# Optimization experiments

Hardware: AMD Instinct MI355X
Metric: run time of the kernel (lower is better)

## Reference

```python
import jax, jax.numpy as jnp
import numpy as np

IN_DIM = 128
D_MODEL = 2 * IN_DIM        # 256, Mamba d_model
D_INNER = 2 * D_MODEL       # 512, expand=2
D_STATE = 16
D_CONV = 4
DT_RANK = (D_MODEL + 15) // 16  # 16
B = 4
C = 1024                    # original channel dim -> Mamba sequence length
EPS = 1e-5


def rmsnorm(x, w):
    return x * jax.lax.rsqrt(jnp.mean(x * x, axis=-1, keepdims=True) + EPS) * w


def conv1x1(x, w, b):
    # x: (B, Cin, L); 1x1 conv == channel matmul
    return jnp.einsum('oi,bil->bol', w, x) + b[None, :, None]


def mamba(u, in_w, conv_w, conv_b, xproj_w, dt_w, dt_b, A_log, Dp, out_w):
    # u: (B, L, D_MODEL) -- faithful mamba_ssm Mamba block (defaults)
    di, K = conv_w.shape
    n = A_log.shape[1]
    r = dt_w.shape[1]
    xz = u @ in_w.T                              # (B,L,2*di)
    xx, z = jnp.split(xz, 2, axis=-1)
    # depthwise causal conv over L
    xt = jnp.pad(jnp.transpose(xx, (0, 2, 1)), ((0, 0), (0, 0), (K - 1, 0)))
    xc = jax.lax.conv_general_dilated(xt, conv_w[:, None, :], (1,), 'VALID',
                                      feature_group_count=di)
    xx = jax.nn.silu(jnp.transpose(xc + conv_b[None, :, None], (0, 2, 1)))
    dbl = xx @ xproj_w.T                         # (B,L,r+2n)
    dt, Bm, Cm = dbl[..., :r], dbl[..., r:r + n], dbl[..., r + n:]
    dt = jax.nn.softplus(dt @ dt_w.T + dt_b)     # (B,L,di)
    A = -jnp.exp(A_log)                          # (di,n)
    dA = jnp.exp(dt[..., None] * A)              # (B,L,di,n)
    dBx = (dt * xx)[..., None] * Bm[:, :, None, :]

    def step(h, inps):
        dA_t, dBx_t, C_t = inps
        h = dA_t * h + dBx_t
        return h, jnp.einsum('bdn,bn->bd', h, C_t)

    h0 = jnp.zeros((u.shape[0], di, n), u.dtype)
    _, ys = jax.lax.scan(step, h0, (jnp.moveaxis(dA, 1, 0),
                                    jnp.moveaxis(dBx, 1, 0),
                                    jnp.moveaxis(Cm, 1, 0)))
    y = jnp.moveaxis(ys, 0, 1) + xx * Dp
    return (y * jax.nn.silu(z)) @ out_w.T


def postnorm_mamba(u, params, norm_w):
    return rmsnorm(mamba(u, *params), norm_w) + u


def _forward(x, W_in, b_in, W_wp, b_wp, W_fp, b_fp, W_bp, b_bp, W_out, b_out,
             norm_w_top,
             f_in_w, f_conv_w, f_conv_b, f_xproj_w, f_dt_w, f_dt_b, f_A_log, f_D, f_out_w, f_norm_w,
             bk_in_w, bk_conv_w, bk_conv_b, bk_xproj_w, bk_dt_w, bk_dt_b, bk_A_log, bk_D, bk_out_w, bk_norm_w):
    residual = x                                  # (B, C, L)
    xn = rmsnorm(x, norm_w_top)                   # RMSNorm over L
    xt = jnp.transpose(xn, (0, 2, 1))             # (B, L, C); L acts as conv channels
    ssm_in = conv1x1(xt, W_in, b_in)              # (B, 2L, C)
    # forward branch
    fwd = conv1x1(ssm_in, W_fp, b_fp)
    fwd = jnp.transpose(fwd, (0, 2, 1))           # (B, C, 2L): Mamba seq=C
    fwd = postnorm_mamba(fwd, (f_in_w, f_conv_w, f_conv_b, f_xproj_w, f_dt_w,
                               f_dt_b, f_A_log, f_D, f_out_w), f_norm_w)
    fwd = jnp.transpose(fwd, (0, 2, 1))           # (B, 2L, C)
    # backward branch (flip along C)
    bwd = conv1x1(ssm_in[:, :, ::-1], W_bp, b_bp)
    bwd = jnp.transpose(bwd, (0, 2, 1))
    bwd = postnorm_mamba(bwd, (bk_in_w, bk_conv_w, bk_conv_b, bk_xproj_w, bk_dt_w,
                               bk_dt_b, bk_A_log, bk_D, bk_out_w), bk_norm_w)
    bwd = jnp.transpose(bwd, (0, 2, 1))[:, :, ::-1]
    # swish gate
    w = conv1x1(xt, W_wp, b_wp)
    w = w * jax.nn.sigmoid(w)
    out = conv1x1(w * fwd + w * bwd, W_out, b_out)  # (B, L, C)
    return jnp.transpose(out, (0, 2, 1)) + residual  # (B, C, L)


def setup_inputs():
    key = jax.random.key(0)
    ks = iter(jax.random.split(key, 64))
    rn = lambda shape, s=0.02: jax.random.normal(next(ks), shape, jnp.float32) * s
    inp = {"x": jax.random.normal(next(ks), (B, C, IN_DIM), jnp.float32)}
    inp["W_in"] = rn((2 * IN_DIM, IN_DIM));   inp["b_in"] = rn((2 * IN_DIM,), 0.1)
    inp["W_wp"] = rn((2 * IN_DIM, IN_DIM));   inp["b_wp"] = rn((2 * IN_DIM,), 0.1)
    inp["W_fp"] = rn((2 * IN_DIM, 2 * IN_DIM)); inp["b_fp"] = rn((2 * IN_DIM,), 0.1)
    inp["W_bp"] = rn((2 * IN_DIM, 2 * IN_DIM)); inp["b_bp"] = rn((2 * IN_DIM,), 0.1)
    inp["W_out"] = rn((IN_DIM, 2 * IN_DIM));  inp["b_out"] = rn((IN_DIM,), 0.1)
    inp["norm_w_top"] = jnp.ones((IN_DIM,), jnp.float32)
    A_init = jnp.log(jnp.broadcast_to(jnp.arange(1, D_STATE + 1, dtype=jnp.float32),
                                      (D_INNER, D_STATE)))
    for p in ("f", "bk"):
        inp[p + "_in_w"] = rn((2 * D_INNER, D_MODEL))
        inp[p + "_conv_w"] = rn((D_INNER, D_CONV), 0.2)
        inp[p + "_conv_b"] = rn((D_INNER,), 0.1)
        inp[p + "_xproj_w"] = rn((DT_RANK + 2 * D_STATE, D_INNER))
        inp[p + "_dt_w"] = rn((D_INNER, DT_RANK), 0.1)
        inp[p + "_dt_b"] = rn((D_INNER,), 0.5)
        inp[p + "_A_log"] = A_init
        inp[p + "_D"] = jnp.ones((D_INNER,), jnp.float32)
        inp[p + "_out_w"] = rn((D_MODEL, D_INNER))
        inp[p + "_norm_w"] = jnp.ones((D_MODEL,), jnp.float32)
    return inp


def reference(x, W_in, b_in, W_wp, b_wp, W_fp, b_fp, W_bp, b_bp, W_out, b_out,
              norm_w_top,
              f_in_w, f_conv_w, f_conv_b, f_xproj_w, f_dt_w, f_dt_b, f_A_log, f_D, f_out_w, f_norm_w,
              bk_in_w, bk_conv_w, bk_conv_b, bk_xproj_w, bk_dt_w, bk_dt_b, bk_A_log, bk_D, bk_out_w, bk_norm_w):
    return _forward(x, W_in, b_in, W_wp, b_wp, W_fp, b_fp, W_bp, b_bp, W_out, b_out,
                    norm_w_top,
                    f_in_w, f_conv_w, f_conv_b, f_xproj_w, f_dt_w, f_dt_b, f_A_log, f_D, f_out_w, f_norm_w,
                    bk_in_w, bk_conv_w, bk_conv_b, bk_xproj_w, bk_dt_w, bk_dt_b, bk_A_log, bk_D, bk_out_w, bk_norm_w)
```

## Files before the change

kernel.cpp:

```cpp
#include <hip/hip_runtime.h>
#include <math.h>

#define C_LEN 1024
#define NROW 4096
#define NCHUNK 32
#define CHUNK 32

typedef __attribute__((ext_vector_type(8))) short short8;
typedef __attribute__((ext_vector_type(4))) float f32x4;

__device__ __forceinline__ float siluf(float x) { return x / (1.f + __expf(-x)); }

__device__ __forceinline__ unsigned short f2bf(float f) {
    unsigned u = __builtin_bit_cast(unsigned, f);
    unsigned r = (u + 0x7FFFu + ((u >> 16) & 1u)) >> 16;
    return (unsigned short)r;
}
__device__ __forceinline__ float bf2f(unsigned short v) {
    unsigned u = ((unsigned)v) << 16;
    return __builtin_bit_cast(float, u);
}

struct WTab {
    const float* s[6];
    unsigned short* d[6];
    int n[6];
};
__global__ __launch_bounds__(256) void k_prep(WTab t, const float* __restrict__ x,
                                              const float* __restrict__ nw,
                                              unsigned short* __restrict__ xn_bf,
                                              const float* __restrict__ W_fp,
                                              const float* __restrict__ W_bp,
                                              const float* __restrict__ W_in,
                                              const float* __restrict__ b_in,
                                              const float* __restrict__ b_fp,
                                              const float* __restrict__ b_bp,
                                              const float* __restrict__ b_wp,
                                              float* __restrict__ Wpin,
                                              float* __restrict__ bmega,
                                              unsigned short* __restrict__ Wmega) {
    int seg = blockIdx.y;
    if (seg < 6) {
        int n = t.n[seg];
        int i = (blockIdx.x * 256 + threadIdx.x) * 4;
        if (i < n) {
            float4 v = *(const float4*)(t.s[seg] + i);
            unsigned short* o = t.d[seg] + i;
            o[0] = f2bf(v.x); o[1] = f2bf(v.y); o[2] = f2bf(v.z); o[3] = f2bf(v.w);
        }
    } else if (seg == 6) {
        int wave = threadIdx.x >> 6, lane = threadIdx.x & 63;
        #pragma unroll
        for (int it = 0; it < 4; ++it) {
            int row = blockIdx.x * 16 + it * 4 + wave;
            if (row < 4096) {
                float2 v = ((const float2*)(x + (size_t)row * 128))[lane];
                float ss = v.x * v.x + v.y * v.y;
                #pragma unroll
                for (int off = 32; off; off >>= 1) ss += __shfl_xor(ss, off, 64);
                float rs = rsqrtf(ss * (1.f / 128.f) + 1e-5f);
                float2 wv = ((const float2*)nw)[lane];
                ushort2 o;
                o.x = f2bf(v.x * rs * wv.x);
                o.y = f2bf(v.y * rs * wv.y);
                ((ushort2*)(xn_bf + (size_t)row * 128))[lane] = o;
            }
        }
    } else {
        int tg = blockIdx.x * 256 + threadIdx.x;
        if (tg < 65536) {
            int p = tg >> 15, rem = tg & 32767;
            int o = rem >> 7, i = rem & 127;
            const float* Wsrc = p ? W_bp : W_fp;
            float s = 0.f;
            #pragma unroll 8
            for (int j = 0; j < 256; ++j) s += Wsrc[o * 256 + j] * W_in[j * 128 + i];
            Wpin[p * 32768 + o * 128 + i] = s;
            Wmega[(size_t)(p * 256 + o) * 128 + i] = f2bf(s);
        } else if (tg < 66048) {
            int q = tg - 65536;
            int p = q >> 8, o = q & 255;
            const float* Wsrc = p ? W_bp : W_fp;
            const float* badd = p ? b_bp : b_fp;
            float s = badd[o];
            #pragma unroll 8
            for (int j = 0; j < 256; ++j) s += Wsrc[o * 256 + j] * b_in[j];
            bmega[p * 256 + o] = s;
        } else if (tg < 66304) {
            int q = tg - 66048;
            bmega[512 + q] = b_wp[q];
        }
    }
}

__global__ __launch_bounds__(256) void k_wcomb2(const float* __restrict__ f_in_w,
                                                const float* __restrict__ bk_in_w,
                                                const float* __restrict__ Wpin,
                                                unsigned short* __restrict__ Wmega,
                                                float* __restrict__ bmega) {
    int tg = blockIdx.x * 256 + threadIdx.x;
    if (tg < 262144) {
        int p = tg >> 17, rem = tg & 131071;
        int o = rem >> 7, i = rem & 127;
        const float* inw = p ? bk_in_w : f_in_w;
        const float* wp = Wpin + p * 32768;
        float s = 0.f;
        #pragma unroll 8
        for (int j = 0; j < 256; ++j) s += inw[o * 256 + j] * wp[j * 128 + i];
        Wmega[(size_t)(768 + p * 1024 + o) * 128 + i] = f2bf(s);
    } else if (tg < 264192) {
        int q = tg - 262144;
        int p = q >> 10, o = q & 1023;
        const float* inw = p ? bk_in_w : f_in_w;
        const float* bp = bmega + p * 256;
        float s = 0.f;
        #pragma unroll 8
        for (int j = 0; j < 256; ++j) s += inw[o * 256 + j] * bp[j];
        bmega[768 + p * 1024 + o] = s;
    }
}

__global__ __launch_bounds__(256) void k_megagemm(const unsigned short* __restrict__ A,
                                                  const unsigned short* __restrict__ W,
                                                  const float* __restrict__ bias,
                                                  unsigned short* __restrict__ uf,
                                                  unsigned short* __restrict__ ub,
                                                  unsigned short* __restrict__ wbuf,
                                                  unsigned short* __restrict__ xzF,
                                                  unsigned short* __restrict__ xzB) {
    __shared__ __align__(16) unsigned short As[128 * 72];
    __shared__ __align__(16) unsigned short Bs[64 * 72];
    const int K = 128;
    int tid = threadIdx.x;
    int m0 = blockIdx.y * 128, n0 = blockIdx.x * 64;
    int w = tid >> 6, lane = tid & 63;
    int q = lane >> 4, ln = lane & 15;

    unsigned short* Cb; int stride, nc0; bool flip = false, dosilu = false;
    if (n0 < 256)       { Cb = uf;   stride = 256;  nc0 = n0; }
    else if (n0 < 512)  { Cb = ub;   stride = 256;  nc0 = n0 - 256;  flip = true; }
    else if (n0 < 768)  { Cb = wbuf; stride = 256;  nc0 = n0 - 512;  dosilu = true; }
    else if (n0 < 1792) { Cb = xzF;  stride = 1024; nc0 = n0 - 768; }
    else                { Cb = xzB;  stride = 1024; nc0 = n0 - 1792; flip = true; }

    int arow0 = tid >> 1;
    int aseg0 = (tid & 1) * 32;
    int brow = tid >> 2, bseg = (tid & 3) * 16;
    const unsigned short* pa = A + (size_t)(m0 + arow0) * K + aseg0;
    const unsigned short* pw = W + (size_t)(n0 + brow) * K + bseg;

    f32x4 acc[2][4];
    #pragma unroll
    for (int i = 0; i < 2; ++i)
        #pragma unroll
        for (int j = 0; j < 4; ++j) acc[i][j] = (f32x4)(0.f);

    for (int k0 = 0; k0 < K; k0 += 64) {
        #pragma unroll
        for (int h = 0; h < 4; ++h)
            *(short8*)&As[arow0 * 72 + aseg0 + h * 8] = *(const short8*)(pa + h * 8);
        *(short8*)&Bs[brow * 72 + bseg]     = *(const short8*)pw;
        *(short8*)&Bs[brow * 72 + bseg + 8] = *(const short8*)(pw + 8);
        pa += 64; pw += 64;
        __syncthreads();
        short8 a0[2], a1[2];
        #pragma unroll
        for (int i = 0; i < 2; ++i) {
            int row = w * 32 + i * 16 + ln;
            a0[i] = *(const short8*)&As[row * 72 + q * 8];
            a1[i] = *(const short8*)&As[row * 72 + 32 + q * 8];
        }
        #pragma unroll
        for (int j = 0; j < 4; ++j) {
            short8 bf0 = *(const short8*)&Bs[(j * 16 + ln) * 72 + q * 8];
            short8 bf1 = *(const short8*)&Bs[(j * 16 + ln) * 72 + 32 + q * 8];
            #pragma unroll
            for (int i = 0; i < 2; ++i) {
                acc[i][j] = __builtin_amdgcn_mfma_f32_16x16x32_bf16(a0[i], bf0, acc[i][j], 0, 0, 0);
                acc[i][j] = __builtin_amdgcn_mfma_f32_16x16x32_bf16(a1[i], bf1, acc[i][j], 0, 0, 0);
            }
        }
        __syncthreads();
    }
    #pragma unroll
    for (int j = 0; j < 4; ++j) {
        float bsv = bias[n0 + j * 16 + ln];
        int nc = nc0 + j * 16 + ln;
        #pragma unroll
        for (int i = 0; i < 2; ++i) {
            #pragma unroll
            for (int r = 0; r < 4; ++r) {
                int m = m0 + w * 32 + i * 16 + q * 4 + r;
                int mw = flip ? (m ^ (C_LEN - 1)) : m;
                float v = acc[i][j][r] + bsv;
                if (dosilu) v = siluf(v);
                Cb[(size_t)mw * stride + nc] = f2bf(v);
            }
        }
    }
}

__global__ __launch_bounds__(256) void k_gemm128(
        const unsigned short* __restrict__ A0, const unsigned short* __restrict__ A1,
        const unsigned short* __restrict__ W0, const unsigned short* __restrict__ W1,
        unsigned short* __restrict__ Cb0, unsigned short* __restrict__ Cb1,
        int N, int K) {
    __shared__ __align__(16) unsigned short As[128 * 72];
    __shared__ __align__(16) unsigned short Bs[64 * 72];
    int p = blockIdx.z;
    const unsigned short* A = p ? A1 : A0;
    const unsigned short* W = p ? W1 : W0;
    unsigned short* Cbf = p ? Cb1 : Cb0;
    int tid = threadIdx.x;
    int m0 = blockIdx.y * 128, n0 = blockIdx.x * 64;
    int w = tid >> 6, lane = tid & 63;
    int q = lane >> 4, ln = lane & 15;

    int arow0 = tid >> 1;
    int aseg0 = (tid & 1) * 32;
    int brow = tid >> 2, bseg = (tid & 3) * 16;
    const unsigned short* pa = A + (size_t)(m0 + arow0) * K + aseg0;
    const unsigned short* pw = W + (size_t)(n0 + brow) * K + bseg;

    f32x4 acc[2][4];
    #pragma unroll
    for (int i = 0; i < 2; ++i)
        #pragma unroll
        for (int j = 0; j < 4; ++j) acc[i][j] = (f32x4)(0.f);

    for (int k0 = 0; k0 < K; k0 += 64) {
        #pragma unroll
        for (int h = 0; h < 4; ++h)
            *(short8*)&As[arow0 * 72 + aseg0 + h * 8] = *(const short8*)(pa + h * 8);
        *(short8*)&Bs[brow * 72 + bseg]     = *(const short8*)pw;
        *(short8*)&Bs[brow * 72 + bseg + 8] = *(const short8*)(pw + 8);
        pa += 64; pw += 64;
        __syncthreads();
        short8 a0[2], a1[2];
        #pragma unroll
        for (int i = 0; i < 2; ++i) {
            int row = w * 32 + i * 16 + ln;
            a0[i] = *(const short8*)&As[row * 72 + q * 8];
            a1[i] = *(const short8*)&As[row * 72 + 32 + q * 8];
        }
        #pragma unroll
        for (int j = 0; j < 4; ++j) {
            short8 bf0 = *(const short8*)&Bs[(j * 16 + ln) * 72 + q * 8];
            short8 bf1 = *(const short8*)&Bs[(j * 16 + ln) * 72 + 32 + q * 8];
            #pragma unroll
            for (int i = 0; i < 2; ++i) {
                acc[i][j] = __builtin_amdgcn_mfma_f32_16x16x32_bf16(a0[i], bf0, acc[i][j], 0, 0, 0);
                acc[i][j] = __builtin_amdgcn_mfma_f32_16x16x32_bf16(a1[i], bf1, acc[i][j], 0, 0, 0);
            }
        }
        __syncthreads();
    }
    #pragma unroll
    for (int i = 0; i < 2; ++i)
        #pragma unroll
        for (int j = 0; j < 4; ++j) {
            int nn = n0 + j * 16 + ln;
            #pragma unroll
            for (int r = 0; r < 4; ++r) {
                int m = m0 + w * 32 + i * 16 + q * 4 + r;
                Cbf[(size_t)m * N + nn] = f2bf(acc[i][j][r]);
            }
        }
}

__global__ __launch_bounds__(256) void k_conv(const unsigned short* __restrict__ xz0,
                                              const unsigned short* __restrict__ xz1,
                                              const float* __restrict__ cw0,
                                              const float* __restrict__ cw1,
                                              const float* __restrict__ cb0,
                                              const float* __restrict__ cb1,
                                              unsigned short* __restrict__ xc0,
                                              unsigned short* __restrict__ xc1) {
    int pz = blockIdx.z;
    const unsigned short* xz = pz ? xz1 : xz0;
    const float* cw = pz ? cw1 : cw0;
    const float* cb = pz ? cb1 : cb0;
    unsigned short* xconv_bf = pz ? xc1 : xc0;
    int d = blockIdx.x * 256 + threadIdx.x;
    int by = blockIdx.y;
    int b = by >> 6, c0 = (by & 63) * 16;
    float4 cwv = *(const float4*)(cw + d * 4);
    float bias = cb[d];
    const unsigned short* base = xz + (size_t)(b * C_LEN) * 1024 + d;
    float w0 = 0.f, w1 = 0.f, w2 = 0.f;
    if (c0) {
        w0 = bf2f(base[(size_t)(c0 - 3) * 1024]);
        w1 = bf2f(base[(size_t)(c0 - 2) * 1024]);
        w2 = bf2f(base[(size_t)(c0 - 1) * 1024]);
    }
    unsigned short* out = xconv_bf + (size_t)(b * C_LEN + c0) * 512 + d;
    #pragma unroll
    for (int i = 0; i < 16; ++i) {
        float cur = bf2f(base[(size_t)(c0 + i) * 1024]);
        float acc = bias;
        acc = fmaf(cwv.x, w0, acc);
        acc = fmaf(cwv.y, w1, acc);
        acc = fmaf(cwv.z, w2, acc);
        acc = fmaf(cwv.w, cur, acc);
        out[(size_t)i * 512] = f2bf(siluf(acc));
        w0 = w1; w1 = w2; w2 = cur;
    }
}

__global__ __launch_bounds__(256) void k_gemm2f_dt(
        const unsigned short* __restrict__ A0, const unsigned short* __restrict__ A1,
        const unsigned short* __restrict__ W0, const unsigned short* __restrict__ W1,
        const float* __restrict__ dtw0, const float* __restrict__ dtw1,
        const float* __restrict__ dtb0, const float* __restrict__ dtb1,
        float* __restrict__ Cf0, float* __restrict__ Cf1,
        unsigned short* __restrict__ dtO0, unsigned short* __restrict__ dtO1) {
    __shared__ __align__(16) unsigned short As[64 * 72];
    __shared__ __align__(16) unsigned short Bs[64 * 72];
    __shared__ float dblS[64][17];
    const int N = 48, K = 512;
    int p = blockIdx.z;
    const unsigned short* A = p ? A1 : A0;
    const unsigned short* W = p ? W1 : W0;
    const float* dtw = p ? dtw1 : dtw0;
    const float* dtb = p ? dtb1 : dtb0;
    float* Cf = p ? Cf1 : Cf0;
    unsigned short* dtO = p ? dtO1 : dtO0;
    int tid = threadIdx.x;
    int m0 = blockIdx.y * 64;
    int w = tid >> 6, lane = tid & 63;
    int q = lane >> 4, ln = lane & 15;
    int srow = tid >> 2;
    int sseg = (tid & 3) * 16;

    const unsigned short* pa = A + (size_t)(m0 + srow) * K + sseg;
    const unsigned short* pw = W + (size_t)srow * K + sseg;
    bool nOK = (srow < N);

    f32x4 acc[4];
    #pragma unroll
    for (int j = 0; j < 4; ++j) acc[j] = (f32x4)(0.f);

    for (int k0 = 0; k0 < K; k0 += 64) {
        *(short8*)&As[srow * 72 + sseg]     = *(const short8*)pa;
        *(short8*)&As[srow * 72 + sseg + 8] = *(const short8*)(pa + 8);
        short8 b0 = (short8)(0), b1 = (short8)(0);
        if (nOK) { b0 = *(const short8*)pw; b1 = *(const short8*)(pw + 8); }
        *(short8*)&Bs[srow * 72 + sseg] = b0;
        *(short8*)&Bs[srow * 72 + sseg + 8] = b1;
        pa += 64; pw += 64;
        __syncthreads();
        short8 af0 = *(const short8*)&As[(w * 16 + ln) * 72 + q * 8];
        short8 af1 = *(const short8*)&As[(w * 16 + ln) * 72 + 32 + q * 8];
        #pragma unroll
        for (int j = 0; j < 4; ++j) {
            short8 bf0 = *(const short8*)&Bs[(j * 16 + ln) * 72 + q * 8];
            short8 bf1 = *(const short8*)&Bs[(j * 16 + ln) * 72 + 32 + q * 8];
            acc[j] = __builtin_amdgcn_mfma_f32_16x16x32_bf16(af0, bf0, acc[j], 0, 0, 0);
            acc[j] = __builtin_amdgcn_mfma_f32_16x16x32_bf16(af1, bf1, acc[j], 0, 0, 0);
        }
        __syncthreads();
    }
    #pragma unroll
    for (int j = 0; j < 4; ++j) {
        int nn = j * 16 + ln;
        #pragma unroll
        for (int r = 0; r < 4; ++r) {
            int mloc = w * 16 + q * 4 + r;
            if (nn < N) Cf[(size_t)(m0 + mloc) * N + nn] = acc[j][r];
            if (j == 0) dblS[mloc][ln] = acc[0][r];
        }
    }
    __syncthreads();
    {
        int dd = tid * 2;
        const float4* wA = (const float4*)(dtw + (size_t)dd * 16);
        float4 a0 = wA[0], a1 = wA[1], a2 = wA[2], a3 = wA[3];
        float4 b0 = wA[4], b1 = wA[5], b2 = wA[6], b3 = wA[7];
        float biasA = dtb[dd], biasB = dtb[dd + 1];
        unsigned short* dto = dtO + (size_t)m0 * 512 + dd;
        for (int row = 0; row < 64; ++row) {
            const float* rv = &dblS[row][0];
            float sA = biasA, sB = biasB;
            sA = fmaf(rv[0], a0.x, sA);  sB = fmaf(rv[0], b0.x, sB);
            sA = fmaf(rv[1], a0.y, sA);  sB = fmaf(rv[1], b0.y, sB);
            sA = fmaf(rv[2], a0.z, sA);  sB = fmaf(rv[2], b0.z, sB);
            sA = fmaf(rv[3], a0.w, sA);  sB = fmaf(rv[3], b0.w, sB);
            sA = fmaf(rv[4], a1.x, sA);  sB = fmaf(rv[4], b1.x, sB);
            sA = fmaf(rv[5], a1.y, sA);  sB = fmaf(rv[5], b1.y, sB);
            sA = fmaf(rv[6], a1.z, sA);  sB = fmaf(rv[6], b1.z, sB);
            sA = fmaf(rv[7], a1.w, sA);  sB = fmaf(rv[7], b1.w, sB);
            sA = fmaf(rv[8], a2.x, sA);  sB = fmaf(rv[8], b2.x, sB);
            sA = fmaf(rv[9], a2.y, sA);  sB = fmaf(rv[9], b2.y, sB);
            sA = fmaf(rv[10], a2.z, sA); sB = fmaf(rv[10], b2.z, sB);
            sA = fmaf(rv[11], a2.w, sA); sB = fmaf(rv[11], b2.w, sB);
            sA = fmaf(rv[12], a3.x, sA); sB = fmaf(rv[12], b3.x, sB);
            sA = fmaf(rv[13], a3.y, sA); sB = fmaf(rv[13], b3.y, sB);
            sA = fmaf(rv[14], a3.z, sA); sB = fmaf(rv[14], b3.z, sB);
            sA = fmaf(rv[15], a3.w, sA); sB = fmaf(rv[15], b3.w, sB);
            float spA = fmaxf(sA, 0.f) + log1pf(__expf(-fabsf(sA)));
            float spB = fmaxf(sB, 0.f) + log1pf(__expf(-fabsf(sB)));
            unsigned pack = (unsigned)f2bf(spA) | ((unsigned)f2bf(spB) << 16);
            *(unsigned*)(dto + (size_t)row * 512) = pack;
        }
    }
}

__global__ __launch_bounds__(256) void k_scan1(const unsigned short* __restrict__ dt0,
                                               const unsigned short* __restrict__ dt1,
                                               const unsigned short* __restrict__ xc0,
                                               const unsigned short* __restrict__ xc1,
                                               const float* __restrict__ dblA,
                                               const float* __restrict__ dblB,
                                               const float* __restrict__ alog0,
                                               const float* __restrict__ alog1,
                                               float* __restrict__ hfin0,
                                               float* __restrict__ hfin1,
                                               float* __restrict__ Pfin0,
                                               float* __restrict__ Pfin1) {
    int z = blockIdx.z;
    int b = z & 3, p = z >> 2;
    const unsigned short* dt = p ? dt1 : dt0;
    const unsigned short* xconv_bf = p ? xc1 : xc0;
    const float* dbl = p ? dblB : dblA;
    const float* A_log = p ? alog1 : alog0;
    float* hfin = p ? hfin1 : hfin0;
    float* Pfin = p ? Pfin1 : Pfin0;
    int tid = threadIdx.x;
    int nh = tid & 1, dl = tid >> 1;
    int k = blockIdx.x, dg = blockIdx.y;
    int d = dg * 128 + dl;
    float4 al0 = *(const float4*)&A_log[d * 16 + nh * 8];
    float4 al1 = *(const float4*)&A_log[d * 16 + nh * 8 + 4];
    float Ac[8] = {-__expf(al0.x), -__expf(al0.y), -__expf(al0.z), -__expf(al0.w),
                   -__expf(al1.x), -__expf(al1.y), -__expf(al1.z), -__expf(al1.w)};
    size_t r0 = (size_t)(b * C_LEN + k * CHUNK);
    const unsigned short* pdt = dt + r0 * 512 + d;
    const unsigned short* pxv = xconv_bf + r0 * 512 + d;
    const float* pB  = dbl + r0 * 48 + 16 + nh * 8;
    float h[8] = {0.f, 0.f, 0.f, 0.f, 0.f, 0.f, 0.f, 0.f};
    float sdt = 0.f;
    #pragma unroll 8
    for (int c = 0; c < CHUNK; ++c) {
        float dtv = bf2f(*pdt);
        float xv  = bf2f(*pxv);
        float4 B0 = *(const float4*)pB;
        float4 B1 = *(const float4*)(pB + 4);
        float dx = dtv * xv;
        float Bv[8] = {B0.x, B0.y, B0.z, B0.w, B1.x, B1.y, B1.z, B1.w};
        #pragma unroll
        for (int j = 0; j < 8; ++j)
            h[j] = fmaf(__expf(dtv * Ac[j]), h[j], dx * Bv[j]);
        sdt += dtv;
        pdt += 512; pxv += 512; pB += 48;
    }
    size_t idx = ((size_t)(b * NCHUNK + k) * 512 + d) * 16 + nh * 8;
    *(float4*)&hfin[idx]     = make_float4(h[0], h[1], h[2], h[3]);
    *(float4*)&hfin[idx + 4] = make_float4(h[4], h[5], h[6], h[7]);
    *(float4*)&Pfin[idx]     = make_float4(__expf(Ac[0] * sdt), __expf(Ac[1] * sdt),
                                           __expf(Ac[2] * sdt), __expf(Ac[3] * sdt));
    *(float4*)&Pfin[idx + 4] = make_float4(__expf(Ac[4] * sdt), __expf(Ac[5] * sdt),
                                           __expf(Ac[6] * sdt), __expf(Ac[7] * sdt));
}

__global__ __launch_bounds__(256) void k_scan2(const float* __restrict__ hfin0,
                                               const float* __restrict__ hfin1,
                                               float* __restrict__ Pfin0,
                                               float* __restrict__ Pfin1) {
    int tt = blockIdx.x * 256 + threadIdx.x;
    int p = tt >> 15;
    int t = tt & 32767;
    const float* hfin = p ? hfin1 : hfin0;
    float* Pfin = p ? Pfin1 : Pfin0;
    int b = t >> 13;
    int dn = t & 8191;
    float carry = 0.f;
    #pragma unroll
    for (int k = 0; k < NCHUNK; ++k) {
        size_t idx = (size_t)(b * NCHUNK + k) * 8192 + dn;
        float pv = Pfin[idx];
        float hf = hfin[idx];
        Pfin[idx] = carry;
        carry = fmaf(pv, carry, hf);
    }
}

__global__ __launch_bounds__(256) void k_scan3(const unsigned short* __restrict__ dt0,
                                               const unsigned short* __restrict__ dt1,
                                               const unsigned short* __restrict__ xc0,
                                               const unsigned short* __restrict__ xc1,
                                               const float* __restrict__ dblA,
                                               const float* __restrict__ dblB,
                                               const unsigned short* __restrict__ xz0,
                                               const unsigned short* __restrict__ xz1,
                                               const float* __restrict__ alog0,
                                               const float* __restrict__ alog1,
                                               const float* __restrict__ Dp0,
                                               const float* __restrict__ Dp1,
                                               const float* __restrict__ carry0,
                                               const float* __restrict__ carry1,
                                               unsigned short* __restrict__ g0,
                                               unsigned short* __restrict__ g1) {
    int z = blockIdx.z;
    int b = z & 3, p = z >> 2;
    const unsigned short* dt = p ? dt1 : dt0;
    const unsigned short* xconv_bf = p ? xc1 : xc0;
    const float* dbl = p ? dblB : dblA;
    const unsigned short* xz = p ? xz1 : xz0;
    const float* A_log = p ? alog1 : alog0;
    const float* Dp = p ? Dp1 : Dp0;
    const float* carryArr = p ? carry1 : carry0;
    unsigned short* gated_bf = p ? g1 : g0;
    int tid = threadIdx.x;
    int nh = tid & 1, dl = tid >> 1;
    int k = blockIdx.x, dg = blockIdx.y;
    int d = dg * 128 + dl;
    float4 al0 = *(const float4*)&A_log[d * 16 + nh * 8];
    float4 al1 = *(const float4*)&A_log[d * 16 + nh * 8 + 4];
    float Ac[8] = {-__expf(al0.x), -__expf(al0.y), -__expf(al0.z), -__expf(al0.w),
                   -__expf(al1.x), -__expf(al1.y), -__expf(al1.z), -__expf(al1.w)};
    float Dd = Dp[d];
    size_t idx = ((size_t)(b * NCHUNK + k) * 512 + d) * 16 + nh * 8;
    float4 h0 = *(const float4*)&carryArr[idx];
    float4 h1 = *(const float4*)&carryArr[idx + 4];
    float h[8] = {h0.x, h0.y, h0.z, h0.w, h1.x, h1.y, h1.z, h1.w};
    size_t r0 = (size_t)(b * C_LEN + k * CHUNK);
    const unsigned short* pdt = dt + r0 * 512 + d;
    const unsigned short* pxv = xconv_bf + r0 * 512 + d;
    const float* pB  = dbl + r0 * 48 + 16 + nh * 8;
    const float* pC  = dbl + r0 * 48 + 32 + nh * 8;
    const unsigned short* pz = xz + r0 * 1024 + 512 + d;
    unsigned short* pg = gated_bf + r0 * 512 + d;
    #pragma unroll 4
    for (int c = 0; c < CHUNK; ++c) {
        float dtv = bf2f(*pdt);
        float xv  = bf2f(*pxv);
        float4 B0 = *(const float4*)pB;
        float4 B1 = *(const float4*)(pB + 4);
        float4 C0 = *(const float4*)pC;
        float4 C1 = *(const float4*)(pC + 4);
        float dx = dtv * xv;
        float Bv[8] = {B0.x, B0.y, B0.z, B0.w, B1.x, B1.y, B1.z, B1.w};
        float Cv[8] = {C0.x, C0.y, C0.z, C0.w, C1.x, C1.y, C1.z, C1.w};
        float contrib = 0.f;
        #pragma unroll
        for (int j = 0; j < 8; ++j) {
            h[j] = fmaf(__expf(dtv * Ac[j]), h[j], dx * Bv[j]);
            contrib = fmaf(h[j], Cv[j], contrib);
        }
        contrib += __shfl_xor(contrib, 1, 64);
        if (nh == 0) {
            float y = contrib + xv * Dd;
            float zv = bf2f(*pz);
            *pg = f2bf(y * siluf(zv));
        }
        pdt += 512; pxv += 512; pB += 48; pC += 48; pz += 1024; pg += 512;
    }
}

__global__ __launch_bounds__(256) void k_outcomb(
        const unsigned short* __restrict__ mo0, const unsigned short* __restrict__ mo1,
        const float* __restrict__ nw0, const float* __restrict__ nw1,
        const unsigned short* __restrict__ uf, const unsigned short* __restrict__ ub,
        const unsigned short* __restrict__ wbuf,
        const unsigned short* __restrict__ W,
        const float* __restrict__ bias,
        const float* __restrict__ resid,
        float* __restrict__ Cf) {
    __shared__ __align__(16) unsigned short As[64 * 264];
    __shared__ __align__(16) unsigned short Bs[128 * 72];
    const int K = 256;
    int tid = threadIdx.x;
    int m0 = blockIdx.x * 64;

    {
        int row = tid >> 2, qq = tid & 3;
        int r = m0 + row;
        int rf = r ^ (C_LEN - 1);
        int c0 = qq * 64;
        const unsigned short* pm0 = mo0 + (size_t)r * 256 + c0;
        const unsigned short* pm1 = mo1 + (size_t)rf * 256 + c0;
        float ss0 = 0.f, ss1 = 0.f;
        #pragma unroll
        for (int c = 0; c < 64; c += 8) {
            short8 v0 = *(const short8*)(pm0 + c);
            short8 v1 = *(const short8*)(pm1 + c);
            #pragma unroll
            for (int j = 0; j < 8; ++j) {
                float f0 = bf2f((unsigned short)v0[j]);
                float f1 = bf2f((unsigned short)v1[j]);
                ss0 = fmaf(f0, f0, ss0);
                ss1 = fmaf(f1, f1, ss1);
            }
        }
        ss0 += __shfl_xor(ss0, 1, 64); ss0 += __shfl_xor(ss0, 2, 64);
        ss1 += __shfl_xor(ss1, 1, 64); ss1 += __shfl_xor(ss1, 2, 64);
        float rs0 = rsqrtf(ss0 * (1.f / 256.f) + 1e-5f);
        float rs1 = rsqrtf(ss1 * (1.f / 256.f) + 1e-5f);
        const unsigned short* pu = uf + (size_t)r * 256 + c0;
        const unsigned short* pb = ub + (size_t)rf * 256 + c0;
        const unsigned short* pwv = wbuf + (size_t)r * 256 + c0;
        #pragma unroll
        for (int c = 0; c < 64; c += 8) {
            short8 v0 = *(const short8*)(pm0 + c);
            short8 v1 = *(const short8*)(pm1 + c);
            short8 vu = *(const short8*)(pu + c);
            short8 vb = *(const short8*)(pb + c);
            short8 vw = *(const short8*)(pwv + c);
            float4 wa0 = *(const float4*)(nw0 + c0 + c);
            float4 wa1 = *(const float4*)(nw0 + c0 + c + 4);
            float4 wb0 = *(const float4*)(nw1 + c0 + c);
            float4 wb1 = *(const float4*)(nw1 + c0 + c + 4);
            float wav[8] = {wa0.x, wa0.y, wa0.z, wa0.w, wa1.x, wa1.y, wa1.z, wa1.w};
            float wbv[8] = {wb0.x, wb0.y, wb0.z, wb0.w, wb1.x, wb1.y, wb1.z, wb1.w};
            short8 o;
            #pragma unroll
            for (int j = 0; j < 8; ++j) {
                float mf = bf2f((unsigned short)v0[j]) * rs0 * wav[j] +
                           bf2f((unsigned short)vu[j]);
                float mb = bf2f((unsigned short)v1[j]) * rs1 * wbv[j] +
                           bf2f((unsigned short)vb[j]);
                o[j] = (short)f2bf(bf2f((unsigned short)vw[j]) * (mf + mb));
            }
            *(short8*)&As[row * 264 + c0 + c] = o;
        }
    }
    __syncthreads();

    int w = tid >> 6, lane = tid & 63;
    int q = lane >> 4, ln = lane & 15;
    int brow = tid >> 1, bseg = (tid & 1) * 32;
    const unsigned short* pw = W + (size_t)brow * K + bseg;

    f32x4 acc[8];
    #pragma unroll
    for (int j = 0; j < 8; ++j) acc[j] = (f32x4)(0.f);

    for (int k0 = 0; k0 < K; k0 += 64) {
        #pragma unroll
        for (int h = 0; h < 4; ++h)
            *(short8*)&Bs[brow * 72 + bseg + h * 8] = *(const short8*)(pw + h * 8);
        pw += 64;
        __syncthreads();
        short8 af0 = *(const short8*)&As[(w * 16 + ln) * 264 + k0 + q * 8];
        short8 af1 = *(const short8*)&As[(w * 16 + ln) * 264 + k0 + 32 + q * 8];
        #pragma unroll
        for (int j = 0; j < 8; ++j) {
            short8 bf0 = *(const short8*)&Bs[(j * 16 + ln) * 72 + q * 8];
            short8 bf1 = *(const short8*)&Bs[(j * 16 + ln) * 72 + 32 + q * 8];
            acc[j] = __builtin_amdgcn_mfma_f32_16x16x32_bf16(af0, bf0, acc[j], 0, 0, 0);
            acc[j] = __builtin_amdgcn_mfma_f32_16x16x32_bf16(af1, bf1, acc[j], 0, 0, 0);
        }
        __syncthreads();
    }
    #pragma unroll
    for (int j = 0; j < 8; ++j) {
        int nn = j * 16 + ln;
        float bsv = bias[nn];
        #pragma unroll
        for (int r = 0; r < 4; ++r) {
            int m = m0 + w * 16 + q * 4 + r;
            Cf[(size_t)m * 128 + nn] = acc[j][r] + bsv + resid[(size_t)m * 128 + nn];
        }
    }
}

extern "C" void kernel_launch(void* const* d_in, const int* in_sizes, int n_in,
                              void* d_out, int out_size, void* d_ws, size_t ws_size,
                              hipStream_t stream) {
    const float* x          = (const float*)d_in[0];
    const float* W_in       = (const float*)d_in[1];
    const float* b_in       = (const float*)d_in[2];
    const float* W_wp       = (const float*)d_in[3];
    const float* b_wp       = (const float*)d_in[4];
    const float* W_fp       = (const float*)d_in[5];
    const float* b_fp       = (const float*)d_in[6];
    const float* W_bp       = (const float*)d_in[7];
    const float* b_bp       = (const float*)d_in[8];
    const float* W_out      = (const float*)d_in[9];
    const float* b_out      = (const float*)d_in[10];
    const float* norm_w_top = (const float*)d_in[11];
    const float* mamba_p[2][10];
    for (int p = 0; p < 2; ++p)
        for (int i = 0; i < 10; ++i)
            mamba_p[p][i] = (const float*)d_in[12 + p * 10 + i];

    float* ws = (float*)d_ws;
    float* dblP[2]  = {ws + 0,       ws + 196608};
    unsigned short* dtsP[2] = {(unsigned short*)(ws + 393216),
                               (unsigned short*)(ws + 2490368)};
    float* Wpin  = ws + 1441792;
    float* bmega = ws + 1507328;
    float* hfinP[2] = {ws + 4587520, ws + 5636096};
    float* PfinP[2] = {ws + 6684672, ws + 7733248};

    unsigned short* us = (unsigned short*)(ws + 8781824);
    unsigned short* xn_bf   = us + 0;
    unsigned short* uf_bf   = us + 1572864;
    unsigned short* ub_bf   = us + 2621440;
    unsigned short* wbuf_bf = us + 3670016;
    unsigned short* xzP[2]  = {us + 4718592,  us + 8912896};
    unsigned short* xcP[2]  = {us + 13107200, us + 15204352};
    unsigned short* gP[2]   = {us + 17301504, us + 19398656};
    unsigned short* moP[2]  = {us + 21495808, us + 22544384};
    unsigned short* Wmega   = us + 23592960;
    unsigned short* wb      = us + 25690112;
    unsigned short* wb_W_out = wb + 196608;
    unsigned short* wb_xp[2]  = {wb + 491520, wb + 909312};
    unsigned short* wb_outw[2]= {wb + 516096, wb + 933888};

    WTab t;
    t.s[0] = W_wp;            t.d[0] = Wmega + 512 * 128; t.n[0] = 32768;
    t.s[1] = W_out;           t.d[1] = wb_W_out;          t.n[1] = 32768;
    t.s[2] = mamba_p[0][3];   t.d[2] = wb_xp[0];          t.n[2] = 24576;
    t.s[3] = mamba_p[0][8];   t.d[3] = wb_outw[0];        t.n[3] = 131072;
    t.s[4] = mamba_p[1][3];   t.d[4] = wb_xp[1];          t.n[4] = 24576;
    t.s[5] = mamba_p[1][8];   t.d[5] = wb_outw[1];        t.n[5] = 131072;
    k_prep<<<dim3(260, 8), 256, 0, stream>>>(t, x, norm_w_top, xn_bf,
                                             W_fp, W_bp, W_in, b_in, b_fp, b_bp, b_wp,
                                             Wpin, bmega, Wmega);
    k_wcomb2<<<1040, 256, 0, stream>>>(mamba_p[0][0], mamba_p[1][0], Wpin, Wmega, bmega);
    k_megagemm<<<dim3(44, 32), 256, 0, stream>>>(xn_bf, Wmega, bmega,
                                                 uf_bf, ub_bf, wbuf_bf, xzP[0], xzP[1]);
    k_conv<<<dim3(2, 256, 2), 256, 0, stream>>>(xzP[0], xzP[1],
                                                mamba_p[0][1], mamba_p[1][1],
                                                mamba_p[0][2], mamba_p[1][2],
                                                xcP[0], xcP[1]);
    k_gemm2f_dt<<<dim3(1, 64, 2), 256, 0, stream>>>(xcP[0], xcP[1], wb_xp[0], wb_xp[1],
                                                    mamba_p[0][4], mamba_p[1][4],
                                                    mamba_p[0][5], mamba_p[1][5],
                                                    dblP[0], dblP[1], dtsP[0], dtsP[1]);
    k_scan1<<<dim3(NCHUNK, 4, 8), 256, 0, stream>>>(dtsP[0], dtsP[1], xcP[0], xcP[1],
                                                    dblP[0], dblP[1],
                                                    mamba_p[0][6], mamba_p[1][6],
                                                    hfinP[0], hfinP[1], PfinP[0], PfinP[1]);
    k_scan2<<<256, 256, 0, stream>>>(hfinP[0], hfinP[1], PfinP[0], PfinP[1]);
    k_scan3<<<dim3(NCHUNK, 4, 8), 256, 0, stream>>>(dtsP[0], dtsP[1], xcP[0], xcP[1],
                                                    dblP[0], dblP[1], xzP[0], xzP[1],
                                                    mamba_p[0][6], mamba_p[1][6],
                                                    mamba_p[0][7], mamba_p[1][7],
                                                    PfinP[0], PfinP[1], gP[0], gP[1]);
    k_gemm128<<<dim3(4, 32, 2), 256, 0, stream>>>(gP[0], gP[1], wb_outw[0], wb_outw[1],
                                                  moP[0], moP[1], 256, 512);
    k_outcomb<<<64, 256, 0, stream>>>(moP[0], moP[1],
                                      mamba_p[0][9], mamba_p[1][9],
                                      uf_bf, ub_bf, wbuf_bf,
                                      wb_W_out, b_out, x, (float*)d_out);
}
```

Before: 304.5 us.

## Shrink row tiles in x-proj/dt and output kernels to launch more blocks

The x-projection plus dt kernel drops its 64-row MFMA tile for 16-row blocks that compute the 48 dbl outputs with scalar bf16 dot products from a shared-memory row tile. The grid grows from 128 to 512 blocks. The output combine kernel likewise moves to 16-row tiles: each wave now handles 32 output columns and the RMS reduction spreads across 16 lanes, raising its grid from 64 to 256 blocks. The aim is to fill the many compute units on the device, at the cost of re-reading weights more often and giving up MFMA in the x-projection.

```diff
diff --git a/kernel.cpp b/kernel.cpp
--- a/kernel.cpp
+++ b/kernel.cpp
@@ -307,70 +307,61 @@
     }
 }
 
-__global__ __launch_bounds__(256) void k_gemm2f_dt(
-        const unsigned short* __restrict__ A0, const unsigned short* __restrict__ A1,
+__global__ __launch_bounds__(256) void k_dbldt(
+        const unsigned short* __restrict__ xcA, const unsigned short* __restrict__ xcB,
         const unsigned short* __restrict__ W0, const unsigned short* __restrict__ W1,
         const float* __restrict__ dtw0, const float* __restrict__ dtw1,
         const float* __restrict__ dtb0, const float* __restrict__ dtb1,
         float* __restrict__ Cf0, float* __restrict__ Cf1,
         unsigned short* __restrict__ dtO0, unsigned short* __restrict__ dtO1) {
-    __shared__ __align__(16) unsigned short As[64 * 72];
-    __shared__ __align__(16) unsigned short Bs[64 * 72];
-    __shared__ float dblS[64][17];
-    const int N = 48, K = 512;
-    int p = blockIdx.z;
-    const unsigned short* A = p ? A1 : A0;
+    __shared__ __align__(16) unsigned short As[16][520];
+    __shared__ float dblS[16][17];
+    int p = blockIdx.y;
+    const unsigned short* xc = p ? xcB : xcA;
     const unsigned short* W = p ? W1 : W0;
     const float* dtw = p ? dtw1 : dtw0;
     const float* dtb = p ? dtb1 : dtb0;
     float* Cf = p ? Cf1 : Cf0;
     unsigned short* dtO = p ? dtO1 : dtO0;
     int tid = threadIdx.x;
-    int m0 = blockIdx.y * 64;
-    int w = tid >> 6, lane = tid & 63;
-    int q = lane >> 4, ln = lane & 15;
-    int srow = tid >> 2;
-    int sseg = (tid & 3) * 16;
-
-    const unsigned short* pa = A + (size_t)(m0 + srow) * K + sseg;
-    const unsigned short* pw = W + (size_t)srow * K + sseg;
-    bool nOK = (srow < N);
-
-    f32x4 acc[4];
-    #pragma unroll
-    for (int j = 0; j < 4; ++j) acc[j] = (f32x4)(0.f);
-
-    for (int k0 = 0; k0 < K; k0 += 64) {
-        *(short8*)&As[srow * 72 + sseg]     = *(const short8*)pa;
-        *(short8*)&As[srow * 72 + sseg + 8] = *(const short8*)(pa + 8);
-        short8 b0 = (short8)(0), b1 = (short8)(0);
-        if (nOK) { b0 = *(const short8*)pw; b1 = *(const short8*)(pw + 8); }
-        *(short8*)&Bs[srow * 72 + sseg] = b0;
-        *(short8*)&Bs[srow * 72 + sseg + 8] = b1;
-        pa += 64; pw += 64;
-        __syncthreads();
-        short8 af0 = *(const short8*)&As[(w * 16 + ln) * 72 + q * 8];
-        short8 af1 = *(const short8*)&As[(w * 16 + ln) * 72 + 32 + q * 8];
-        #pragma unroll
-        for (int j = 0; j < 4; ++j) {
-            short8 bf0 = *(const short8*)&Bs[(j * 16 + ln) * 72 + q * 8];
-            short8 bf1 = *(const short8*)&Bs[(j * 16 + ln) * 72 + 32 + q * 8];
-            acc[j] = __builtin_amdgcn_mfma_f32_16x16x32_bf16(af0, bf0, acc[j], 0, 0, 0);
-            acc[j] = __builtin_amdgcn_mfma_f32_16x16x32_bf16(af1, bf1, acc[j], 0, 0, 0);
-        }
-        __syncthreads();
-    }
-    #pragma unroll
-    for (int j = 0; j < 4; ++j) {
-        int nn = j * 16 + ln;
-        #pragma unroll
-        for (int r = 0; r < 4; ++r) {
-            int mloc = w * 16 + q * 4 + r;
-            if (nn < N) Cf[(size_t)(m0 + mloc) * N + nn] = acc[j][r];
-            if (j == 0) dblS[mloc][ln] = acc[0][r];
-        }
+    int m0 = blockIdx.x * 16;
+
+    {
+        int r = tid >> 4, cc = (tid & 15) * 32;
+        const unsigned short* src = xc + (size_t)(m0 + r) * 512 + cc;
+        #pragma unroll
+        for (int i = 0; i < 4; ++i)
+            *(short8*)&As[r][cc + i * 8] = *(const short8*)(src + i * 8);
     }
     __syncthreads();
+
+    {
+        int r = tid >> 4, c0 = tid & 15;
+        const unsigned short* w0p = W + (size_t)c0 * 512;
+        const unsigned short* w1p = W + (size_t)(c0 + 16) * 512;
+        const unsigned short* w2p = W + (size_t)(c0 + 32) * 512;
+        float s0 = 0.f, s1 = 0.f, s2 = 0.f;
+        for (int k = 0; k < 512; k += 8) {
+            short8 a8 = *(const short8*)&As[r][k];
+            short8 b0 = *(const short8*)(w0p + k);
+            short8 b1 = *(const short8*)(w1p + k);
+            short8 b2 = *(const short8*)(w2p + k);
+            #pragma unroll
+            for (int j = 0; j < 8; ++j) {
+                float av = bf2f((unsigned short)a8[j]);
+                s0 = fmaf(av, bf2f((unsigned short)b0[j]), s0);
+                s1 = fmaf(av, bf2f((unsigned short)b1[j]), s1);
+                s2 = fmaf(av, bf2f((unsigned short)b2[j]), s2);
+            }
+        }
+        float* Crow = Cf + (size_t)(m0 + r) * 48;
+        Crow[c0] = s0;
+        Crow[c0 + 16] = s1;
+        Crow[c0 + 32] = s2;
+        dblS[r][c0] = s0;
+    }
+    __syncthreads();
+
     {
         int dd = tid * 2;
         const float4* wA = (const float4*)(dtw + (size_t)dd * 16);
@@ -378,7 +369,8 @@
         float4 b0 = wA[4], b1 = wA[5], b2 = wA[6], b3 = wA[7];
         float biasA = dtb[dd], biasB = dtb[dd + 1];
         unsigned short* dto = dtO + (size_t)m0 * 512 + dd;
-        for (int row = 0; row < 64; ++row) {
+        #pragma unroll 4
+        for (int row = 0; row < 16; ++row) {
             const float* rv = &dblS[row][0];
             float sA = biasA, sB = biasB;
             sA = fmaf(rv[0], a0.x, sA);  sB = fmaf(rv[0], b0.x, sB);
@@ -566,22 +558,22 @@
         const float* __restrict__ bias,
         const float* __restrict__ resid,
         float* __restrict__ Cf) {
-    __shared__ __align__(16) unsigned short As[64 * 264];
+    __shared__ __align__(16) unsigned short As[16 * 264];
     __shared__ __align__(16) unsigned short Bs[128 * 72];
     const int K = 256;
     int tid = threadIdx.x;
-    int m0 = blockIdx.x * 64;
+    int m0 = blockIdx.x * 16;
 
     {
-        int row = tid >> 2, qq = tid & 3;
+        int row = tid >> 4, qq = tid & 15;
         int r = m0 + row;
         int rf = r ^ (C_LEN - 1);
-        int c0 = qq * 64;
+        int c0 = qq * 16;
         const unsigned short* pm0 = mo0 + (size_t)r * 256 + c0;
         const unsigned short* pm1 = mo1 + (size_t)rf * 256 + c0;
         float ss0 = 0.f, ss1 = 0.f;
         #pragma unroll
-        for (int c = 0; c < 64; c += 8) {
+        for (int c = 0; c < 16; c += 8) {
             short8 v0 = *(const short8*)(pm0 + c);
             short8 v1 = *(const short8*)(pm1 + c);
             #pragma unroll
@@ -592,15 +584,17 @@
                 ss1 = fmaf(f1, f1, ss1);
             }
         }
-        ss0 += __shfl_xor(ss0, 1, 64); ss0 += __shfl_xor(ss0, 2, 64);
-        ss1 += __shfl_xor(ss1, 1, 64); ss1 += __shfl_xor(ss1, 2, 64);
+        ss0 += __shfl_xor(ss0, 1, 64); ss1 += __shfl_xor(ss1, 1, 64);
+        ss0 += __shfl_xor(ss0, 2, 64); ss1 += __shfl_xor(ss1, 2, 64);
+        ss0 += __shfl_xor(ss0, 4, 64); ss1 += __shfl_xor(ss1, 4, 64);
+        ss0 += __shfl_xor(ss0, 8, 64); ss1 += __shfl_xor(ss1, 8, 64);
         float rs0 = rsqrtf(ss0 * (1.f / 256.f) + 1e-5f);
         float rs1 = rsqrtf(ss1 * (1.f / 256.f) + 1e-5f);
         const unsigned short* pu = uf + (size_t)r * 256 + c0;
         const unsigned short* pb = ub + (size_t)rf * 256 + c0;
         const unsigned short* pwv = wbuf + (size_t)r * 256 + c0;
         #pragma unroll
-        for (int c = 0; c < 64; c += 8) {
+        for (int c = 0; c < 16; c += 8) {
             short8 v0 = *(const short8*)(pm0 + c);
             short8 v1 = *(const short8*)(pm1 + c);
             short8 vu = *(const short8*)(pu + c);
@@ -631,9 +625,9 @@
     int brow = tid >> 1, bseg = (tid & 1) * 32;
     const unsigned short* pw = W + (size_t)brow * K + bseg;
 
-    f32x4 acc[8];
-    #pragma unroll
-    for (int j = 0; j < 8; ++j) acc[j] = (f32x4)(0.f);
+    f32x4 acc[2];
+    acc[0] = (f32x4)(0.f);
+    acc[1] = (f32x4)(0.f);
 
     for (int k0 = 0; k0 < K; k0 += 64) {
         #pragma unroll
@@ -641,24 +635,24 @@
             *(short8*)&Bs[brow * 72 + bseg + h * 8] = *(const short8*)(pw + h * 8);
         pw += 64;
         __syncthreads();
-        short8 af0 = *(const short8*)&As[(w * 16 + ln) * 264 + k0 + q * 8];
-        short8 af1 = *(const short8*)&As[(w * 16 + ln) * 264 + k0 + 32 + q * 8];
-        #pragma unroll
-        for (int j = 0; j < 8; ++j) {
-            short8 bf0 = *(const short8*)&Bs[(j * 16 + ln) * 72 + q * 8];
-            short8 bf1 = *(const short8*)&Bs[(j * 16 + ln) * 72 + 32 + q * 8];
+        short8 af0 = *(const short8*)&As[ln * 264 + k0 + q * 8];
+        short8 af1 = *(const short8*)&As[ln * 264 + k0 + 32 + q * 8];
+        #pragma unroll
+        for (int j = 0; j < 2; ++j) {
+            short8 bf0 = *(const short8*)&Bs[(w * 32 + j * 16 + ln) * 72 + q * 8];
+            short8 bf1 = *(const short8*)&Bs[(w * 32 + j * 16 + ln) * 72 + 32 + q * 8];
             acc[j] = __builtin_amdgcn_mfma_f32_16x16x32_bf16(af0, bf0, acc[j], 0, 0, 0);
             acc[j] = __builtin_amdgcn_mfma_f32_16x16x32_bf16(af1, bf1, acc[j], 0, 0, 0);
         }
         __syncthreads();
     }
     #pragma unroll
-    for (int j = 0; j < 8; ++j) {
-        int nn = j * 16 + ln;
+    for (int j = 0; j < 2; ++j) {
+        int nn = w * 32 + j * 16 + ln;
         float bsv = bias[nn];
         #pragma unroll
         for (int r = 0; r < 4; ++r) {
-            int m = m0 + w * 16 + q * 4 + r;
+            int m = m0 + q * 4 + r;
             Cf[(size_t)m * 128 + nn] = acc[j][r] + bsv + resid[(size_t)m * 128 + nn];
         }
     }
@@ -725,10 +719,10 @@
                                                 mamba_p[0][1], mamba_p[1][1],
                                                 mamba_p[0][2], mamba_p[1][2],
                                                 xcP[0], xcP[1]);
-    k_gemm2f_dt<<<dim3(1, 64, 2), 256, 0, stream>>>(xcP[0], xcP[1], wb_xp[0], wb_xp[1],
-                                                    mamba_p[0][4], mamba_p[1][4],
-                                                    mamba_p[0][5], mamba_p[1][5],
-                                                    dblP[0], dblP[1], dtsP[0], dtsP[1]);
+    k_dbldt<<<dim3(256, 2), 256, 0, stream>>>(xcP[0], xcP[1], wb_xp[0], wb_xp[1],
+                                              mamba_p[0][4], mamba_p[1][4],
+                                              mamba_p[0][5], mamba_p[1][5],
+                                              dblP[0], dblP[1], dtsP[0], dtsP[1]);
     k_scan1<<<dim3(NCHUNK, 4, 8), 256, 0, stream>>>(dtsP[0], dtsP[1], xcP[0], xcP[1],
                                                     dblP[0], dblP[1],
                                                     mamba_p[0][6], mamba_p[1][6],
@@ -741,8 +735,8 @@
                                                     PfinP[0], PfinP[1], gP[0], gP[1]);
     k_gemm128<<<dim3(4, 32, 2), 256, 0, stream>>>(gP[0], gP[1], wb_outw[0], wb_outw[1],
                                                   moP[0], moP[1], 256, 512);
-    k_outcomb<<<64, 256, 0, stream>>>(moP[0], moP[1],
-                                      mamba_p[0][9], mamba_p[1][9],
-                                      uf_bf, ub_bf, wbuf_bf,
-                                      wb_W_out, b_out, x, (float*)d_out);
-}
+    k_outcomb<<<256, 256, 0, stream>>>(moP[0], moP[1],
+                                       mamba_p[0][9], mamba_p[1][9],
+                                       uf_bf, ub_bf, wbuf_bf,
+                                       wb_W_out, b_out, x, (float*)d_out);
+}
```

New measurement: 312.4 us. +2.6%, slower.
